# Kernel tuning notes

Hardware: AMD Instinct MI355X
Metric: run time of the kernel (lower is better)

Reference implementation:

```python
import jax, jax.numpy as jnp
import numpy as np

B_SZ, L_SEQ, H_CH, N_ST = 8, 4096, 256, 64


def setup_inputs() -> dict:
    key = jax.random.key(0)
    ks = jax.random.split(key, 12)
    rn = lambda k, s, sc=1.0: jax.random.normal(k, s, jnp.float32) * sc
    inp = {
        'x': rn(ks[0], (B_SZ, L_SEQ, H_CH)),
        # stable DPLR spectrum: Re(Lambda) < 0, HiPPO-like imaginary ladder
        'Lambda_re': -(jnp.abs(rn(ks[1], (N_ST,))) + 0.1),
        'Lambda_im': jnp.pi * jnp.arange(N_ST, dtype=jnp.float32),
        'P_re': rn(ks[2], (N_ST,), N_ST ** -0.5),
        'P_im': rn(ks[3], (N_ST,), N_ST ** -0.5),
        'Q_re': rn(ks[4], (N_ST,), N_ST ** -0.5),
        'Q_im': rn(ks[5], (N_ST,), N_ST ** -0.5),
        'B_re': rn(ks[6], (N_ST,), N_ST ** -0.5),
        'B_im': rn(ks[7], (N_ST,), N_ST ** -0.5),
        'C_re': rn(ks[8], (H_CH, N_ST), N_ST ** -0.5),
        'C_im': rn(ks[9], (H_CH, N_ST), N_ST ** -0.5),
        'step': jnp.ones((1,), jnp.float32) * 1e-3,
        'D': jnp.zeros((1,), jnp.float32),
        'W_fc': rn(ks[10], (H_CH, H_CH), H_CH ** -0.5),
        'b_fc': jnp.zeros((H_CH,), jnp.float32),
        'ln_g': jnp.ones((H_CH,), jnp.float32),
        'ln_b': jnp.zeros((H_CH,), jnp.float32),
    }
    return inp


def _dplr_kernel(Lambda_re, Lambda_im, P_re, P_im, Q_re, Q_im, B_re, B_im, C_re, C_im, step, L):
    # S4 DPLR generating function evaluated at the L roots of unity (torch_get_K_derta).
    Lam = (Lambda_re + 1j * Lambda_im).astype(jnp.complex64)  # (N,)
    Pc = (P_re + 1j * P_im).astype(jnp.complex64)
    Qc = (Q_re + 1j * Q_im).astype(jnp.complex64)
    Bc = (B_re + 1j * B_im).astype(jnp.complex64)
    Cc = (C_re + 1j * C_im).astype(jnp.complex64)  # (H, N)
    k = jnp.arange(L, dtype=jnp.float32)
    Omega = jnp.exp((-2j * jnp.pi) * (k / L)).astype(jnp.complex64)  # (L,)
    c = 2.0 / (1.0 + Omega)
    g = (2.0 / step[0]) * (1.0 - Omega) / (1.0 + Omega)  # bilinear transform points, (L,)
    inv = 1.0 / (g[:, None] - Lam[None, :])  # Cauchy matrix, (L, N)
    k00 = jnp.einsum('hn,ln->hl', Cc * Bc[None, :], inv)  # (H, L)
    k01 = jnp.einsum('hn,ln->hl', Cc * Pc[None, :], inv)
    k10 = jnp.einsum('n,ln->l', Qc * Bc, inv)  # (L,)
    k11 = jnp.einsum('n,ln->l', Qc * Pc, inv)
    atRoots = c[None, :] * (k00 - k01 * (k10 / (1.0 + k11))[None, :])  # Woodbury correction
    K = jnp.fft.ifft(atRoots, axis=-1).real  # (H, L)
    return K.astype(jnp.float32)


def reference(x, Lambda_re, Lambda_im, P_re, P_im, Q_re, Q_im, B_re, B_im, C_re, C_im, step, D, W_fc, b_fc, ln_g, ln_b):
    Bsz, L, H = x.shape
    step = jnp.maximum(step, 1e-6)
    K = _dplr_kernel(Lambda_re, Lambda_im, P_re, P_im, Q_re, Q_im, B_re, B_im, C_re, C_im, step, L)  # (H, L)
    # causal FFT convolution per channel (torch_convolution with fft=True)
    n = 2 * L
    Kf = jnp.fft.rfft(K, n=n, axis=-1)           # (H, F)
    uf = jnp.fft.rfft(x, n=n, axis=1)            # (B, F, H)
    h1 = jnp.fft.irfft(uf * Kf.T[None], n=n, axis=1)[:, :L, :]
    y1 = jax.nn.gelu(h1 + D * x, approximate=False)  # mult_activation='gelu'
    y2 = jax.nn.gelu(y1 @ W_fc.T + b_fc, approximate=False)  # fc + final_act
    y2 = y2 + x  # skip
    mu = jnp.mean(y2, axis=-1, keepdims=True)
    var = jnp.var(y2, axis=-1, keepdims=True)
    y = (y2 - mu) / jnp.sqrt(var + 1e-5) * ln_g + ln_b  # LayerNorm; dropout p=0
    h_ratio = jnp.max(jnp.abs(y), axis=1) / (jnp.max(jnp.abs(x), axis=1) + 1e-6)  # (B, H)
    return y, h_ratio
```

## Files before the change

kernel.cpp:

```cpp
#include <hip/hip_runtime.h>
#include <math.h>

#define TPB 256

typedef float2 cf;
typedef __attribute__((ext_vector_type(8))) short bf16x8;
typedef __attribute__((ext_vector_type(4))) float f32x4;

__device__ __forceinline__ cf cmk(float x, float y){ cf r; r.x=x; r.y=y; return r; }
__device__ __forceinline__ cf cml(cf a, cf b){ return cmk(a.x*b.x - a.y*b.y, a.x*b.y + a.y*b.x); }
__device__ __forceinline__ cf cad(cf a, cf b){ return cmk(a.x+b.x, a.y+b.y); }
__device__ __forceinline__ cf csb(cf a, cf b){ return cmk(a.x-b.x, a.y-b.y); }
__device__ __forceinline__ cf crcp(cf d){ float r = 1.0f/(d.x*d.x + d.y*d.y); return cmk(d.x*r, -d.y*r); }
__device__ __forceinline__ cf cdv(cf n, cf d){ return cml(n, crcp(d)); }
__device__ __forceinline__ float geluf(float z){ return 0.5f*z*(1.0f + erff(z*0.70710678118654752f)); }

__device__ __forceinline__ cf twid(float f, float sign){
  float h = f * 0.5f;
  float s = __builtin_amdgcn_sinf(h);
  float c0 = __builtin_amdgcn_cosf(h);
  return cmk(c0, sign * s);
}

__device__ __forceinline__ cf shflx(cf v, int m){
  return cmk(__shfl_xor(v.x, m), __shfl_xor(v.y, m));
}

__device__ __forceinline__ void bfsplit(float v, ushort* h, ushort* l){
  unsigned u = __float_as_uint(v);
  unsigned hr = (u + 0x7FFFu + ((u >> 16) & 1u)) & 0xFFFF0000u;
  *h = (ushort)(hr >> 16);
  float lv = v - __uint_as_float(hr);
  unsigned u2 = __float_as_uint(lv);
  *l = (ushort)((u2 + 0x7FFFu + ((u2 >> 16) & 1u)) >> 16);
}

__device__ __forceinline__ void dif4q(cf& q0, cf& q1, cf& q2, cf& q3, cf w1, float sign){
  cf w2 = cml(w1, w1);
  cf a1 = cad(q0, q2);
  cf c1 = cml(csb(q0, q2), w1);
  cf b1 = cad(q1, q3);
  cf d1 = cml(csb(q1, q3), cmk(-sign*w1.y, sign*w1.x));
  q0 = cad(a1, b1);
  q1 = cml(csb(a1, b1), w2);
  q2 = cad(c1, d1);
  q3 = cml(csb(c1, d1), w2);
}
__device__ __forceinline__ void dit4q(cf& q0, cf& q1, cf& q2, cf& q3, cf w1, float sign){
  cf w2 = cml(w1, w1);
  cf t1 = cml(q1, w2);
  cf a1 = cad(q0, t1), b1 = csb(q0, t1);
  cf t2 = cml(q3, w2);
  cf c1 = cad(q2, t2), d1 = csb(q2, t2);
  cf v1 = cml(c1, w1);
  cf v2 = cml(d1, cmk(-sign*w1.y, sign*w1.x));
  q0 = cad(a1, v1);
  q2 = csb(a1, v1);
  q1 = cad(b1, v2);
  q3 = csb(b1, v2);
}

template<int N, int SSTART>
__device__ void fft_dif_r4(cf* __restrict__ a, float sign){
  #pragma unroll
  for (int s = SSTART; s >= 1; s >>= 2){
    __syncthreads();
    #pragma unroll
    for (int g = 0; g < (N >> 2) / TPB; g++){
      int w = (int)threadIdx.x + g * TPB;
      int j = w & (s - 1);
      int base = ((w & ~(s - 1)) << 2) | j;
      cf A0 = a[base], B0 = a[base + s], C0 = a[base + 2*s], D0 = a[base + 3*s];
      cf w1 = twid((float)j / (float)(2 * s), sign);
      cf w2 = cml(w1, w1);
      cf a1 = cad(A0, C0);
      cf c1 = cml(csb(A0, C0), w1);
      cf b1 = cad(B0, D0);
      cf d1 = cml(csb(B0, D0), cmk(-sign * w1.y, sign * w1.x));
      a[base]         = cad(a1, b1);
      a[base + s]     = cml(csb(a1, b1), w2);
      a[base + 2*s]   = cad(c1, d1);
      a[base + 3*s]   = cml(csb(c1, d1), w2);
    }
  }
  if constexpr ((__builtin_ctz(N) & 1) == 1){
    __syncthreads();
    #pragma unroll
    for (int g = 0; g < (N >> 1) / TPB; g++){
      int w = (int)threadIdx.x + g * TPB;
      int i = w << 1;
      cf u = a[i], v = a[i + 1];
      a[i] = cad(u, v);
      a[i + 1] = csb(u, v);
    }
  }
  __syncthreads();
}

template<int N>
__device__ void fft_dit_r4(cf* __restrict__ a, float sign){
  if constexpr ((__builtin_ctz(N) & 1) == 1){
    __syncthreads();
    #pragma unroll
    for (int g = 0; g < (N >> 1) / TPB; g++){
      int w = (int)threadIdx.x + g * TPB;
      int i = w << 1;
      cf u = a[i], v = a[i + 1];
      a[i] = cad(u, v);
      a[i + 1] = csb(u, v);
    }
  }
  constexpr int S0 = ((__builtin_ctz(N) & 1) == 1) ? 2 : 1;
  #pragma unroll
  for (int s = S0; s <= (N >> 2); s <<= 2){
    __syncthreads();
    #pragma unroll
    for (int g = 0; g < (N >> 2) / TPB; g++){
      int w = (int)threadIdx.x + g * TPB;
      int j = w & (s - 1);
      int base = ((w & ~(s - 1)) << 2) | j;
      cf A0 = a[base], B0 = a[base + s], C0 = a[base + 2*s], D0 = a[base + 3*s];
      cf w1 = twid((float)j / (float)(2 * s), sign);
      cf w2 = cml(w1, w1);
      cf t1 = cml(B0, w2);
      cf a1 = cad(A0, t1), b1 = csb(A0, t1);
      cf t2 = cml(D0, w2);
      cf c1 = cad(C0, t2), d1 = csb(C0, t2);
      cf v1 = cml(c1, w1);
      cf v2 = cml(d1, cmk(-sign * w1.y, sign * w1.x));
      a[base]         = cad(a1, v1);
      a[base + 2*s]   = csb(a1, v1);
      a[base + s]     = cad(b1, v2);
      a[base + 3*s]   = csb(b1, v2);
    }
  }
  __syncthreads();
}

__device__ void dif8192_pad_stage(cf* __restrict__ a, float sign){
  __syncthreads();
  #pragma unroll
  for (int g = 0; g < 8; g++){
    int w = (int)threadIdx.x + g * TPB;
    cf A0 = a[w], B0 = a[w + 2048];
    cf w1 = twid((float)w * (1.0f / 4096.0f), sign);
    cf w2 = cml(w1, w1);
    cf c1 = cml(A0, w1);
    cf d1 = cml(B0, cmk(-sign * w1.y, sign * w1.x));
    a[w]        = cad(A0, B0);
    a[w + 2048] = cml(csb(A0, B0), w2);
    a[w + 4096] = cad(c1, d1);
    a[w + 6144] = cml(csb(c1, d1), w2);
  }
}

__device__ __forceinline__ int brev13(int x){ return (int)(__brev((unsigned)x) >> 19); }

__global__ void k_init(unsigned* xmax, unsigned* ymax){
  int i = blockIdx.x * 256 + threadIdx.x;
  if (i < 2048){ xmax[i] = 0u; ymax[i] = 0u; }
}

__global__ __launch_bounds__(256) void k_transpose_x(const float* __restrict__ x,
                                                     float* __restrict__ xT,
                                                     unsigned* __restrict__ xmax){
  __shared__ float tile[64][65];
  __shared__ float red[64][4];
  int b = blockIdx.z;
  int t0 = blockIdx.x * 64;
  int h0 = blockIdx.y * 64;
  int hc = threadIdx.x & 63, tg = threadIdx.x >> 6;
  float pmax = 0.0f;
  #pragma unroll
  for (int q = 0; q < 16; q++){
    int tr = tg + q * 4;
    float v = x[((size_t)(b * 4096 + t0 + tr)) * 256 + h0 + hc];
    tile[tr][hc] = v;
    pmax = fmaxf(pmax, fabsf(v));
  }
  red[hc][tg] = pmax;
  __syncthreads();
  if (threadIdx.x < 64){
    float m = fmaxf(fmaxf(red[threadIdx.x][0], red[threadIdx.x][1]),
                    fmaxf(red[threadIdx.x][2], red[threadIdx.x][3]));
    atomicMax(&xmax[b * 256 + h0 + threadIdx.x], __float_as_uint(m));
  }
  #pragma unroll
  for (int q = 0; q < 16; q++){
    int hr = tg + q * 4;
    xT[((size_t)(b * 256 + h0 + hr)) * 4096 + t0 + hc] = tile[hc][hr];
  }
}

__global__ void k_wsplit(const float* __restrict__ W, ushort* __restrict__ Wh, ushort* __restrict__ Wl){
  int i = blockIdx.x * 256 + threadIdx.x;
  ushort h, l;
  bfsplit(W[i], &h, &l);
  Wh[i] = h; Wl[i] = l;
}

__global__ __launch_bounds__(256) void k_cauchy(
    const float* __restrict__ Lr, const float* __restrict__ Li,
    const float* __restrict__ Pr, const float* __restrict__ Pi,
    const float* __restrict__ Qr, const float* __restrict__ Qi,
    const float* __restrict__ Br, const float* __restrict__ Bi,
    const float* __restrict__ Cr, const float* __restrict__ Ci,
    const float* __restrict__ stepp, cf* __restrict__ A)
{
  __shared__ cf sLam[64], sB[64], sP[64], sQB[64], sQP[64];
  __shared__ cf sInv[64][16];
  __shared__ cf sWood[16], sC[16], sG[16];
  int tid = threadIdx.x;
  int l0 = blockIdx.x * 16;
  float stepv = fmaxf(stepp[0], 1e-6f);
  if (tid < 64){
    cf lam = cmk(Lr[tid], Li[tid]);
    cf b = cmk(Br[tid], Bi[tid]);
    cf p = cmk(Pr[tid], Pi[tid]);
    cf q = cmk(Qr[tid], Qi[tid]);
    sLam[tid] = lam; sB[tid] = b; sP[tid] = p;
    sQB[tid] = cml(q, b);
    sQP[tid] = cml(q, p);
  }
  __syncthreads();
  if (tid < 16){
    int l = l0 + tid;
    float ang = -6.2831855f * ((float)l * (1.0f / 4096.0f));
    cf Om = cmk(cosf(ang), sinf(ang));
    cf den = cmk(1.0f + Om.x, Om.y);
    cf num = cmk(1.0f - Om.x, -Om.y);
    cf rden = crcp(den);
    sC[tid] = cml(cmk(2.0f, 0.0f), rden);
    cf g = cml(num, rden);
    float sc = 2.0f / stepv;
    sG[tid] = cmk(g.x * sc, g.y * sc);
  }
  __syncthreads();
  for (int it = tid; it < 1024; it += 256){
    int n = it >> 4, ll = it & 15;
    sInv[n][ll] = crcp(csb(sG[ll], sLam[n]));
  }
  __syncthreads();
  if (tid < 16){
    cf k10 = cmk(0,0), k11 = cmk(0,0);
    for (int n = 0; n < 64; n++){
      k10 = cad(k10, cml(sQB[n], sInv[n][tid]));
      k11 = cad(k11, cml(sQP[n], sInv[n][tid]));
    }
    sWood[tid] = cdv(k10, cmk(1.0f + k11.x, k11.y));
  }
  __syncthreads();
  int h = tid;
  cf a0[16], a1[16];
  #pragma unroll
  for (int ll = 0; ll < 16; ll++){ a0[ll] = cmk(0,0); a1[ll] = cmk(0,0); }
  for (int n = 0; n < 64; n++){
    cf cc = cmk(Cr[h * 64 + n], Ci[h * 64 + n]);
    cf cb = cml(cc, sB[n]);
    cf cp = cml(cc, sP[n]);
    #pragma unroll
    for (int ll = 0; ll < 16; ll++){
      cf iv = sInv[n][ll];
      a0[ll] = cad(a0[ll], cml(cb, iv));
      a1[ll] = cad(a1[ll], cml(cp, iv));
    }
  }
  cf* dst = A + (size_t)h * 4096 + l0;
  #pragma unroll
  for (int ll = 0; ll < 16; ll++){
    dst[ll] = cml(sC[ll], csb(a0[ll], cml(a1[ll], sWood[ll])));
  }
}

__global__ __launch_bounds__(256) void k_kf(const cf* __restrict__ A, float4* __restrict__ Sab){
  extern __shared__ cf c[];
  int hp = blockIdx.x, tid = threadIdx.x;
  const cf* a1p = A + (size_t)(2 * hp) * 4096;
  const cf* a2p = a1p + 4096;
  for (int l = tid; l < 4096; l += TPB){
    int r = (int)(__brev((unsigned)l) >> 20);
    cf u = a1p[l], v = a2p[l];
    c[r] = cmk(u.x - v.y, u.y + v.x);
  }
  fft_dit_r4<4096>(c, 1.0f);
  float k1[16], k2[16];
  #pragma unroll
  for (int q = 0; q < 16; q++){
    cf w = c[tid + q * 256];
    k1[q] = w.x * (1.0f / 4096.0f);
    k2[q] = w.y * (1.0f / 4096.0f);
  }
  __syncthreads();
  #pragma unroll
  for (int q = 0; q < 16; q++) c[tid + q * 256] = cmk(k1[q], k2[q]);
  dif8192_pad_stage(c, -1.0f);
  fft_dif_r4<8192, 512>(c, -1.0f);
  float4* rec = Sab + (size_t)hp * 4097;
  const float sc = 0.5f * 0.5f * (1.0f / 8192.0f);
  #pragma unroll
  for (int q8 = 0; q8 < 16; q8++){
    int t = tid + 256 * q8;
    int p = t << 1;
    int k = brev13(p);
    int qq = brev13((8192 - k) & 8191);
    cf Zp = c[p], Zq = c[qq];
    float K1x = (Zp.x + Zq.x), K1y = (Zp.y - Zq.y);
    float dx  = (Zp.x - Zq.x), dy  = (Zp.y + Zq.y);
    float K2x = dy, K2y = -dx;
    rec[t] = make_float4((K1x + K2x) * sc, (K1y + K2y) * sc,
                         (K1x - K2x) * sc, (K1y - K2y) * sc);
  }
  if (tid == 0){
    cf Z1 = c[1];
    float K1x = 2.0f * Z1.x, K2x = 2.0f * Z1.y;
    rec[4096] = make_float4((K1x + K2x) * sc, 0.0f, (K1x - K2x) * sc, 0.0f);
  }
}

__global__ __launch_bounds__(256) void k_conv(const float* __restrict__ xT,
                                              const float4* __restrict__ Sab,
                                              const float* __restrict__ Dp,
                                              ushort* __restrict__ y1h,
                                              ushort* __restrict__ y1l){
  __shared__ cf c[8320];
  int blk = blockIdx.x;
  int b = blk >> 7, hp = blk & 127;
  int t = threadIdx.x;
  const float* xs1 = xT + ((size_t)(b * 256 + 2 * hp)) * 4096;
  const float* xs2 = xs1 + 4096;
  cf v[32];
  #pragma unroll
  for (int r = 0; r < 16; r++){
    int n = t + 256 * r;
    v[r] = cmk(xs1[n], xs2[n]);
  }
  #pragma unroll
  for (int r = 0; r < 16; r++)
    v[r + 16] = cml(v[r], twid((float)(t + 256 * r) * (1.0f / 4096.0f), -1.0f));
  #pragma unroll
  for (int r0 = 0; r0 < 4; r0++){
    cf w1 = twid((float)(t + 256 * r0) * (1.0f / 2048.0f), -1.0f);
    dif4q(v[r0], v[r0 + 4], v[r0 + 8], v[r0 + 12], w1, -1.0f);
    dif4q(v[r0 + 16], v[r0 + 20], v[r0 + 24], v[r0 + 28], w1, -1.0f);
  }
  {
    cf w1 = twid((float)t * (1.0f / 512.0f), -1.0f);
    #pragma unroll
    for (int r = 0; r < 32; r += 4)
      dif4q(v[r], v[r + 1], v[r + 2], v[r + 3], w1, -1.0f);
  }
  #pragma unroll
  for (int r = 0; r < 32; r++) c[t + 260 * r] = v[r];
  __syncthreads();
  int Bq = t >> 3, sg = t & 7;
  int m1 = Bq * 260 + sg;
  #pragma unroll
  for (int u = 0; u < 32; u++) v[u] = c[m1 + 8 * u];
  #pragma unroll
  for (int u = 0; u < 8; u++){
    cf w1 = twid((float)(sg + 8 * u) * (1.0f / 128.0f), -1.0f);
    dif4q(v[u], v[u + 8], v[u + 16], v[u + 24], w1, -1.0f);
  }
  #pragma unroll
  for (int p2 = 0; p2 < 2; p2++){
    cf w1 = twid((float)(sg + 8 * p2) * (1.0f / 32.0f), -1.0f);
    #pragma unroll
    for (int u0 = 0; u0 < 32; u0 += 8)
      dif4q(v[u0 + p2], v[u0 + p2 + 2], v[u0 + p2 + 4], v[u0 + p2 + 6], w1, -1.0f);
  }
  {
    cf tw = twid((float)sg * (1.0f / 8.0f), -1.0f);
    #pragma unroll
    for (int u = 0; u < 32; u += 2){
      cf lo = cad(v[u], v[u + 1]);
      cf hi = cml(csb(v[u], v[u + 1]), tw);
      v[u] = lo; v[u + 1] = hi;
    }
  }
  {
    bool h4 = (sg & 4) != 0;
    cf tw4 = twid((float)(sg & 3) * 0.25f, -1.0f);
    #pragma unroll
    for (int u = 0; u < 32; u++){
      cf o = shflx(v[u], 4);
      v[u] = h4 ? cml(csb(o, v[u]), tw4) : cad(v[u], o);
    }
    bool h2 = (sg & 2) != 0;
    cf tw2 = twid((float)(sg & 1) * 0.5f, -1.0f);
    #pragma unroll
    for (int u = 0; u < 32; u++){
      cf o = shflx(v[u], 2);
      v[u] = h2 ? cml(csb(o, v[u]), tw2) : cad(v[u], o);
    }
    bool h1 = (sg & 1) != 0;
    #pragma unroll
    for (int u = 0; u < 32; u++){
      cf o = shflx(v[u], 1);
      v[u] = h1 ? csb(o, v[u]) : cad(v[u], o);
    }
  }
  #pragma unroll
  for (int u = 0; u < 32; u++) c[m1 + 8 * u] = v[u];
  __syncthreads();
  const float4* rec = Sab + (size_t)hp * 4097;
  #pragma unroll
  for (int q8 = 0; q8 < 16; q8++){
    int th = t + 256 * q8;
    int p = th << 1;
    int k = brev13(p);
    int qq = brev13((8192 - k) & 8191);
    int pi = p + 4 * (p >> 8), qi = qq + 4 * (qq >> 8);
    cf Zp = c[pi], Zq = c[qi];
    float4 r0 = rec[th];
    cf Sap = cmk(r0.x, r0.y), Sbp = cmk(r0.z, r0.w);
    cf cZq = cmk(Zq.x, -Zq.y), cZp = cmk(Zp.x, -Zp.y);
    c[pi] = cad(cml(Zp, Sap), cml(cZq, Sbp));
    cf cSa = cmk(Sap.x, -Sap.y), cSb = cmk(Sbp.x, -Sbp.y);
    c[qi] = cad(cml(Zq, cSa), cml(cZp, cSb));
  }
  if (t == 0){
    float4 e = rec[4096];
    cf Z1 = c[1];
    c[1] = cad(cml(Z1, cmk(e.x, e.y)), cml(cmk(Z1.x, -Z1.y), cmk(e.z, e.w)));
  }
  __syncthreads();
  #pragma unroll
  for (int u = 0; u < 32; u++) v[u] = c[m1 + 8 * u];
  {
    bool h1 = (sg & 1) != 0;
    #pragma unroll
    for (int u = 0; u < 32; u++){
      cf o = shflx(v[u], 1);
      v[u] = h1 ? csb(o, v[u]) : cad(v[u], o);
    }
    bool h2 = (sg & 2) != 0;
    cf w2 = twid((float)(sg & 1) * 0.5f, 1.0f);
    #pragma unroll
    for (int u = 0; u < 32; u++){
      cf o = shflx(v[u], 2);
      cf whv = cml(w2, h2 ? v[u] : o);
      v[u] = h2 ? csb(o, whv) : cad(v[u], whv);
    }
    bool h4 = (sg & 4) != 0;
    cf w4 = twid((float)(sg & 3) * 0.25f, 1.0f);
    #pragma unroll
    for (int u = 0; u < 32; u++){
      cf o = shflx(v[u], 4);
      cf whv = cml(w4, h4 ? v[u] : o);
      v[u] = h4 ? csb(o, whv) : cad(v[u], whv);
    }
  }
  {
    cf tw = twid((float)sg * (1.0f / 8.0f), 1.0f);
    #pragma unroll
    for (int u = 0; u < 32; u += 2){
      cf tb = cml(v[u + 1], tw);
      cf a = v[u];
      v[u] = cad(a, tb);
      v[u + 1] = csb(a, tb);
    }
  }
  #pragma unroll
  for (int p2 = 0; p2 < 2; p2++){
    cf w1 = twid((float)(sg + 8 * p2) * (1.0f / 32.0f), 1.0f);
    #pragma unroll
    for (int u0 = 0; u0 < 32; u0 += 8)
      dit4q(v[u0 + p2], v[u0 + p2 + 2], v[u0 + p2 + 4], v[u0 + p2 + 6], w1, 1.0f);
  }
  #pragma unroll
  for (int u = 0; u < 8; u++){
    cf w1 = twid((float)(sg + 8 * u) * (1.0f / 128.0f), 1.0f);
    dit4q(v[u], v[u + 8], v[u + 16], v[u + 24], w1, 1.0f);
  }
  #pragma unroll
  for (int u = 0; u < 32; u++) c[m1 + 8 * u] = v[u];
  __syncthreads();
  #pragma unroll
  for (int r = 0; r < 32; r++) v[r] = c[t + 260 * r];
  {
    cf tw = twid((float)t * (1.0f / 256.0f), 1.0f);
    #pragma unroll
    for (int r = 0; r < 32; r += 2){
      cf tb = cml(v[r + 1], tw);
      cf a = v[r];
      v[r] = cad(a, tb);
      v[r + 1] = csb(a, tb);
    }
  }
  #pragma unroll
  for (int p2 = 0; p2 < 2; p2++){
    cf w1 = twid((float)(t + 256 * p2) * (1.0f / 1024.0f), 1.0f);
    #pragma unroll
    for (int r0 = 0; r0 < 32; r0 += 8)
      dit4q(v[r0 + p2], v[r0 + p2 + 2], v[r0 + p2 + 4], v[r0 + p2 + 6], w1, 1.0f);
  }
  #pragma unroll
  for (int r0 = 0; r0 < 8; r0++){
    cf w1 = twid((float)(t + 256 * r0) * (1.0f / 4096.0f), 1.0f);
    dit4q(v[r0], v[r0 + 8], v[r0 + 16], v[r0 + 24], w1, 1.0f);
  }
  float Dv = Dp[0];
  size_t base = ((size_t)(b * 256 + 2 * hp)) * 4096;
  #pragma unroll
  for (int r = 0; r < 16; r++){
    int n = t + 256 * r;
    cf w = v[r];
    float z1 = geluf(fmaf(Dv, xs1[n], w.x));
    float z2 = geluf(fmaf(Dv, xs2[n], w.y));
    ushort h0, l0, h1u, l1;
    bfsplit(z1, &h0, &l0);
    bfsplit(z2, &h1u, &l1);
    y1h[base + n] = h0;        y1l[base + n] = l0;
    y1h[base + 4096 + n] = h1u; y1l[base + 4096 + n] = l1;
  }
}

__global__ __launch_bounds__(256, 3) void k_gemm_ln(
    const ushort* __restrict__ y1h, const ushort* __restrict__ y1l,
    const ushort* __restrict__ Wh, const ushort* __restrict__ Wl,
    const float* __restrict__ bfc, const float* __restrict__ x,
    const float* __restrict__ lng, const float* __restrict__ lnb,
    float* __restrict__ yout, unsigned* __restrict__ ymax)
{
  __shared__ ushort sY[2][64 * 40];
  __shared__ float red1[64][4], red2[64][4];
  int tid = threadIdx.x;
  int l = tid & 63;
  int w = tid >> 6;
  int blk = blockIdx.x;
  int b = blk >> 6;
  int t0 = (blk & 63) * 64;
  int g = l >> 4, cc = l & 15;

  f32x4 acc[4][4];
  #pragma unroll
  for (int m = 0; m < 4; m++)
    #pragma unroll
    for (int n = 0; n < 4; n++)
      acc[m][n] = (f32x4){0.0f, 0.0f, 0.0f, 0.0f};

  int kk = tid >> 3, ts = (tid & 7) * 8;

  #pragma unroll 1
  for (int kc = 0; kc < 256; kc += 32){
    __syncthreads();
    {
      size_t gb = ((size_t)(b * 256 + kc + kk)) * 4096 + t0 + ts;
      float4 vh = *(const float4*)(y1h + gb);
      float4 vl = *(const float4*)(y1l + gb);
      const ushort* ph = (const ushort*)&vh;
      const ushort* pl = (const ushort*)&vl;
      int kblk = kk >> 3, kin = kk & 7;
      #pragma unroll
      for (int e = 0; e < 8; e++){
        int t = ts + e;
        int idx = t * 40 + ((kblk ^ ((t >> 3) & 3)) << 3) + kin;
        sY[0][idx] = ph[e];
        sY[1][idx] = pl[e];
      }
    }
    __syncthreads();
    bf16x8 afh[4], afl[4];
    #pragma unroll
    for (int m = 0; m < 4; m++){
      int t = m * 16 + cc;
      int idx = t * 40 + ((g ^ ((t >> 3) & 3)) << 3);
      afh[m] = *(bf16x8*)&sY[0][idx];
      afl[m] = *(bf16x8*)&sY[1][idx];
    }
    #pragma unroll
    for (int n = 0; n < 4; n++){
      size_t wj = (size_t)(w * 64 + n * 16 + cc) * 256 + kc + g * 8;
      bf16x8 bh = *(const bf16x8*)(Wh + wj);
      bf16x8 bl = *(const bf16x8*)(Wl + wj);
      #pragma unroll
      for (int m = 0; m < 4; m++){
        acc[m][n] = __builtin_amdgcn_mfma_f32_16x16x32_bf16(afh[m], bh, acc[m][n], 0, 0, 0);
        acc[m][n] = __builtin_amdgcn_mfma_f32_16x16x32_bf16(afh[m], bl, acc[m][n], 0, 0, 0);
        acc[m][n] = __builtin_amdgcn_mfma_f32_16x16x32_bf16(afl[m], bh, acc[m][n], 0, 0, 0);
      }
    }
  }

  float bj[4], gj[4], lj[4];
  #pragma unroll
  for (int n = 0; n < 4; n++){
    int j = w * 64 + n * 16 + cc;
    bj[n] = bfc[j]; gj[n] = lng[j]; lj[n] = lnb[j];
  }
  #pragma unroll
  for (int m = 0; m < 4; m++){
    #pragma unroll
    for (int r = 0; r < 4; r++){
      int tl = m * 16 + g * 4 + r;
      size_t rowb = ((size_t)(b * 4096 + t0 + tl)) * 256;
      float ss = 0.0f, sq = 0.0f;
      #pragma unroll
      for (int n = 0; n < 4; n++){
        float z = geluf(acc[m][n][r] + bj[n]) + x[rowb + w * 64 + n * 16 + cc];
        acc[m][n][r] = z;
        ss += z; sq = fmaf(z, z, sq);
      }
      #pragma unroll
      for (int msk = 1; msk < 16; msk <<= 1){
        ss += __shfl_xor(ss, msk);
        sq += __shfl_xor(sq, msk);
      }
      if (cc == 0){ red1[tl][w] = ss; red2[tl][w] = sq; }
    }
  }
  __syncthreads();
  float jm[4] = {0.0f, 0.0f, 0.0f, 0.0f};
  #pragma unroll
  for (int m = 0; m < 4; m++){
    #pragma unroll
    for (int r = 0; r < 4; r++){
      int tl = m * 16 + g * 4 + r;
      float ts1 = red1[tl][0] + red1[tl][1] + red1[tl][2] + red1[tl][3];
      float ts2 = red2[tl][0] + red2[tl][1] + red2[tl][2] + red2[tl][3];
      float mu = ts1 * (1.0f / 256.0f);
      float var = ts2 * (1.0f / 256.0f) - mu * mu;
      float rstd = rsqrtf(var + 1e-5f);
      size_t rowb = ((size_t)(b * 4096 + t0 + tl)) * 256;
      #pragma unroll
      for (int n = 0; n < 4; n++){
        float yv = (acc[m][n][r] - mu) * rstd * gj[n] + lj[n];
        yout[rowb + w * 64 + n * 16 + cc] = yv;
        jm[n] = fmaxf(jm[n], fabsf(yv));
      }
    }
  }
  #pragma unroll
  for (int n = 0; n < 4; n++){
    jm[n] = fmaxf(jm[n], __shfl_xor(jm[n], 16));
    jm[n] = fmaxf(jm[n], __shfl_xor(jm[n], 32));
  }
  if (g == 0){
    #pragma unroll
    for (int n = 0; n < 4; n++)
      atomicMax(&ymax[b * 256 + w * 64 + n * 16 + cc], __float_as_uint(jm[n]));
  }
}

__global__ void k_ratio(const unsigned* __restrict__ ymax, const unsigned* __restrict__ xmax,
                        float* __restrict__ out){
  int i = blockIdx.x * 256 + threadIdx.x;
  if (i < 2048){
    float ym = __uint_as_float(ymax[i]);
    float xm = __uint_as_float(xmax[i]);
    out[8388608 + i] = ym / (xm + 1e-6f);
  }
}

extern "C" void kernel_launch(void* const* d_in, const int* in_sizes, int n_in,
                              void* d_out, int out_size, void* d_ws, size_t ws_size,
                              hipStream_t stream)
{
  const float* x    = (const float*)d_in[0];
  const float* Lr   = (const float*)d_in[1];
  const float* Li   = (const float*)d_in[2];
  const float* Pr   = (const float*)d_in[3];
  const float* Pi   = (const float*)d_in[4];
  const float* Qr   = (const float*)d_in[5];
  const float* Qi   = (const float*)d_in[6];
  const float* Br   = (const float*)d_in[7];
  const float* Bi   = (const float*)d_in[8];
  const float* Cr   = (const float*)d_in[9];
  const float* Ci   = (const float*)d_in[10];
  const float* stp  = (const float*)d_in[11];
  const float* Dp   = (const float*)d_in[12];
  const float* Wfc  = (const float*)d_in[13];
  const float* bfc  = (const float*)d_in[14];
  const float* lng  = (const float*)d_in[15];
  const float* lnb  = (const float*)d_in[16];

  char* ws = (char*)d_ws;
  float*    xT   = (float*)(ws);
  float4*   Sab  = (float4*)(ws + ((size_t)32 << 20));
  cf*       A    = (cf*)(ws + ((size_t)41 << 20));
  ushort*   y1h  = (ushort*)(ws + ((size_t)41 << 20));
  ushort*   y1l  = (ushort*)(ws + ((size_t)57 << 20));
  ushort*   Wh   = (ushort*)(ws + ((size_t)73 << 20));
  ushort*   Wl   = (ushort*)(ws + ((size_t)73 << 20) + (128u << 10));
  unsigned* xmax = (unsigned*)(ws + ((size_t)73 << 20) + (256u << 10));
  unsigned* ymax = xmax + 2048;

  k_init<<<8, 256, 0, stream>>>(xmax, ymax);
  dim3 gt(64, 4, 8);
  k_transpose_x<<<gt, 256, 0, stream>>>(x, xT, xmax);
  k_wsplit<<<256, 256, 0, stream>>>(Wfc, Wh, Wl);
  k_cauchy<<<256, 256, 0, stream>>>(Lr, Li, Pr, Pi, Qr, Qi, Br, Bi, Cr, Ci, stp, A);
  k_kf<<<128, 256, 65536, stream>>>(A, Sab);
  k_conv<<<1024, 256, 0, stream>>>(xT, Sab, Dp, y1h, y1l);
  k_gemm_ln<<<512, 256, 0, stream>>>(y1h, y1l, Wh, Wl, bfc, x, lng, lnb, (float*)d_out, ymax);
  k_ratio<<<8, 256, 0, stream>>>(ymax, xmax, (float*)d_out);
}
```

Baseline: 211.2 us.

## Split 8192-point padded FFT convolution into even/odd 4096-point halves

The convolution replaces the single 8192-point zero-padded FFT per channel pair with two 4096-point FFTs: one for the even frequency bins and one for the twiddled odd bins. The kernel spectra for the two halves are computed separately (S0 directly from the Cauchy values, Tt via a twiddled 4096 FFT), and the two inverse results are summed with an output twiddle. This halves the shared-memory footprint and register array per block so more blocks can be resident, at the cost of an extra kernel launch and two sequential smaller FFT passes.

Result: slower. 375.4 us (+77.8%).

```diff
diff --git a/kernel.cpp b/kernel.cpp
--- a/kernel.cpp
+++ b/kernel.cpp
@@ -11,6 +11,7 @@
 __device__ __forceinline__ cf cml(cf a, cf b){ return cmk(a.x*b.x - a.y*b.y, a.x*b.y + a.y*b.x); }
 __device__ __forceinline__ cf cad(cf a, cf b){ return cmk(a.x+b.x, a.y+b.y); }
 __device__ __forceinline__ cf csb(cf a, cf b){ return cmk(a.x-b.x, a.y-b.y); }
+__device__ __forceinline__ cf cjg(cf a){ return cmk(a.x, -a.y); }
 __device__ __forceinline__ cf crcp(cf d){ float r = 1.0f/(d.x*d.x + d.y*d.y); return cmk(d.x*r, -d.y*r); }
 __device__ __forceinline__ cf cdv(cf n, cf d){ return cml(n, crcp(d)); }
 __device__ __forceinline__ float geluf(float z){ return 0.5f*z*(1.0f + erff(z*0.70710678118654752f)); }
@@ -137,24 +138,137 @@
   __syncthreads();
 }
 
-__device__ void dif8192_pad_stage(cf* __restrict__ a, float sign){
-  __syncthreads();
-  #pragma unroll
-  for (int g = 0; g < 8; g++){
-    int w = (int)threadIdx.x + g * TPB;
-    cf A0 = a[w], B0 = a[w + 2048];
-    cf w1 = twid((float)w * (1.0f / 4096.0f), sign);
-    cf w2 = cml(w1, w1);
-    cf c1 = cml(A0, w1);
-    cf d1 = cml(B0, cmk(-sign * w1.y, sign * w1.x));
-    a[w]        = cad(A0, B0);
-    a[w + 2048] = cml(csb(A0, B0), w2);
-    a[w + 4096] = cad(c1, d1);
-    a[w + 6144] = cml(csb(c1, d1), w2);
-  }
-}
-
-__device__ __forceinline__ int brev13(int x){ return (int)(__brev((unsigned)x) >> 19); }
+__device__ __forceinline__ int brev12(int x){ return (int)(__brev((unsigned)x) >> 20); }
+
+
+__device__ __forceinline__ void dif4096_reg(cf (&v)[16], cf* __restrict__ c, int t, int lo){
+  #pragma unroll
+  for (int r0 = 0; r0 < 4; r0++){
+    cf w1 = twid((float)(t + 256*r0) * (1.0f/2048.0f), -1.0f);
+    dif4q(v[r0], v[r0+4], v[r0+8], v[r0+12], w1, -1.0f);
+  }
+  {
+    cf w1 = twid((float)t * (1.0f/512.0f), -1.0f);
+    #pragma unroll
+    for (int g = 0; g < 16; g += 4)
+      dif4q(v[g], v[g+1], v[g+2], v[g+3], w1, -1.0f);
+  }
+  __syncthreads();
+  #pragma unroll
+  for (int r = 0; r < 16; r++) c[t + 260*r] = v[r];
+  __syncthreads();
+  int m1 = (t >> 4) * 260 + lo;
+  #pragma unroll
+  for (int u = 0; u < 16; u++) v[u] = c[m1 + 16*u];
+  #pragma unroll
+  for (int u0 = 0; u0 < 4; u0++){
+    cf w1 = twid((float)(16*u0 + lo) * (1.0f/128.0f), -1.0f);
+    dif4q(v[u0], v[u0+4], v[u0+8], v[u0+12], w1, -1.0f);
+  }
+  {
+    cf w1 = twid((float)lo * (1.0f/32.0f), -1.0f);
+    #pragma unroll
+    for (int g = 0; g < 16; g += 4)
+      dif4q(v[g], v[g+1], v[g+2], v[g+3], w1, -1.0f);
+  }
+  {
+    bool h8 = (lo & 8) != 0;
+    cf tw8 = twid((float)(lo & 7) * 0.125f, -1.0f);
+    #pragma unroll
+    for (int u = 0; u < 16; u++){
+      cf o = shflx(v[u], 8);
+      v[u] = h8 ? cml(csb(o, v[u]), tw8) : cad(v[u], o);
+    }
+    bool h4 = (lo & 4) != 0;
+    cf tw4 = twid((float)(lo & 3) * 0.25f, -1.0f);
+    #pragma unroll
+    for (int u = 0; u < 16; u++){
+      cf o = shflx(v[u], 4);
+      v[u] = h4 ? cml(csb(o, v[u]), tw4) : cad(v[u], o);
+    }
+    bool h2 = (lo & 2) != 0;
+    cf tw2 = twid((float)(lo & 1) * 0.5f, -1.0f);
+    #pragma unroll
+    for (int u = 0; u < 16; u++){
+      cf o = shflx(v[u], 2);
+      v[u] = h2 ? cml(csb(o, v[u]), tw2) : cad(v[u], o);
+    }
+    bool h1 = (lo & 1) != 0;
+    #pragma unroll
+    for (int u = 0; u < 16; u++){
+      cf o = shflx(v[u], 1);
+      v[u] = h1 ? csb(o, v[u]) : cad(v[u], o);
+    }
+  }
+  #pragma unroll
+  for (int u = 0; u < 16; u++) c[m1 + 16*u] = v[u];
+  __syncthreads();
+}
+
+__device__ __forceinline__ void dit4096_reg(cf (&v)[16], cf* __restrict__ c, int t, int lo){
+  int m1 = (t >> 4) * 260 + lo;
+  #pragma unroll
+  for (int u = 0; u < 16; u++) v[u] = c[m1 + 16*u];
+  {
+    bool h1 = (lo & 1) != 0;
+    #pragma unroll
+    for (int u = 0; u < 16; u++){
+      cf o = shflx(v[u], 1);
+      v[u] = h1 ? csb(o, v[u]) : cad(v[u], o);
+    }
+    bool h2 = (lo & 2) != 0;
+    cf w2 = twid((float)(lo & 1) * 0.5f, 1.0f);
+    #pragma unroll
+    for (int u = 0; u < 16; u++){
+      cf o = shflx(v[u], 2);
+      cf whv = cml(w2, h2 ? v[u] : o);
+      v[u] = h2 ? csb(o, whv) : cad(v[u], whv);
+    }
+    bool h4 = (lo & 4) != 0;
+    cf w4 = twid((float)(lo & 3) * 0.25f, 1.0f);
+    #pragma unroll
+    for (int u = 0; u < 16; u++){
+      cf o = shflx(v[u], 4);
+      cf whv = cml(w4, h4 ? v[u] : o);
+      v[u] = h4 ? csb(o, whv) : cad(v[u], whv);
+    }
+    bool h8 = (lo & 8) != 0;
+    cf w8 = twid((float)(lo & 7) * 0.125f, 1.0f);
+    #pragma unroll
+    for (int u = 0; u < 16; u++){
+      cf o = shflx(v[u], 8);
+      cf whv = cml(w8, h8 ? v[u] : o);
+      v[u] = h8 ? csb(o, whv) : cad(v[u], whv);
+    }
+  }
+  {
+    cf w1 = twid((float)lo * (1.0f/32.0f), 1.0f);
+    #pragma unroll
+    for (int g = 0; g < 16; g += 4)
+      dit4q(v[g], v[g+1], v[g+2], v[g+3], w1, 1.0f);
+  }
+  #pragma unroll
+  for (int u0 = 0; u0 < 4; u0++){
+    cf w1 = twid((float)(16*u0 + lo) * (1.0f/128.0f), 1.0f);
+    dit4q(v[u0], v[u0+4], v[u0+8], v[u0+12], w1, 1.0f);
+  }
+  #pragma unroll
+  for (int u = 0; u < 16; u++) c[m1 + 16*u] = v[u];
+  __syncthreads();
+  #pragma unroll
+  for (int r = 0; r < 16; r++) v[r] = c[t + 260*r];
+  {
+    cf w1 = twid((float)t * (1.0f/512.0f), 1.0f);
+    #pragma unroll
+    for (int g = 0; g < 16; g += 4)
+      dit4q(v[g], v[g+1], v[g+2], v[g+3], w1, 1.0f);
+  }
+  #pragma unroll
+  for (int r0 = 0; r0 < 4; r0++){
+    cf w1 = twid((float)(t + 256*r0) * (1.0f/2048.0f), 1.0f);
+    dit4q(v[r0], v[r0+4], v[r0+8], v[r0+12], w1, 1.0f);
+  }
+}
 
 __global__ void k_init(unsigned* xmax, unsigned* ymax){
   int i = blockIdx.x * 256 + threadIdx.x;
@@ -272,245 +386,140 @@
   }
 }
 
-__global__ __launch_bounds__(256) void k_kf(const cf* __restrict__ A, float4* __restrict__ Sab){
+__global__ __launch_bounds__(256) void k_s0(const cf* __restrict__ A, float4* __restrict__ S0){
+  int hp = blockIdx.x;
+  int rec = blockIdx.y * 256 + threadIdx.x;
+  if (rec > 2048) return;
+  int k = (rec < 2048) ? brev12(rec << 1) : 2048;
+  int mk = (4096 - k) & 4095;
+  const cf* a1p = A + (size_t)(2 * hp) * 4096;
+  const cf* a2p = a1p + 4096;
+  cf K1 = cad(a1p[k], cjg(a1p[mk]));
+  cf K2 = cad(a2p[k], cjg(a2p[mk]));
+  const float s = 1.0f / 32768.0f;
+  S0[(size_t)hp * 2049 + rec] = make_float4((K1.x + K2.x) * s, (K1.y + K2.y) * s,
+                                            (K1.x - K2.x) * s, (K1.y - K2.y) * s);
+}
+
+__global__ __launch_bounds__(256) void k_kf(const cf* __restrict__ A, float4* __restrict__ Tt){
   extern __shared__ cf c[];
   int hp = blockIdx.x, tid = threadIdx.x;
   const cf* a1p = A + (size_t)(2 * hp) * 4096;
   const cf* a2p = a1p + 4096;
   for (int l = tid; l < 4096; l += TPB){
-    int r = (int)(__brev((unsigned)l) >> 20);
-    cf u = a1p[l], v = a2p[l];
-    c[r] = cmk(u.x - v.y, u.y + v.x);
+    int r = brev12(l);
+    cf u = a1p[l], w = a2p[l];
+    c[r] = cmk(u.x - w.y, u.y + w.x);
   }
   fft_dit_r4<4096>(c, 1.0f);
-  float k1[16], k2[16];
-  #pragma unroll
-  for (int q = 0; q < 16; q++){
-    cf w = c[tid + q * 256];
-    k1[q] = w.x * (1.0f / 4096.0f);
-    k2[q] = w.y * (1.0f / 4096.0f);
-  }
-  __syncthreads();
-  #pragma unroll
-  for (int q = 0; q < 16; q++) c[tid + q * 256] = cmk(k1[q], k2[q]);
-  dif8192_pad_stage(c, -1.0f);
-  fft_dif_r4<8192, 512>(c, -1.0f);
-  float4* rec = Sab + (size_t)hp * 4097;
-  const float sc = 0.5f * 0.5f * (1.0f / 8192.0f);
-  #pragma unroll
-  for (int q8 = 0; q8 < 16; q8++){
-    int t = tid + 256 * q8;
-    int p = t << 1;
-    int k = brev13(p);
-    int qq = brev13((8192 - k) & 8191);
-    cf Zp = c[p], Zq = c[qq];
-    float K1x = (Zp.x + Zq.x), K1y = (Zp.y - Zq.y);
-    float dx  = (Zp.x - Zq.x), dy  = (Zp.y + Zq.y);
-    float K2x = dy, K2y = -dx;
-    rec[t] = make_float4((K1x + K2x) * sc, (K1y + K2y) * sc,
-                         (K1x - K2x) * sc, (K1y - K2y) * sc);
-  }
-  if (tid == 0){
-    cf Z1 = c[1];
-    float K1x = 2.0f * Z1.x, K2x = 2.0f * Z1.y;
-    rec[4096] = make_float4((K1x + K2x) * sc, 0.0f, (K1x - K2x) * sc, 0.0f);
-  }
-}
-
-__global__ __launch_bounds__(256) void k_conv(const float* __restrict__ xT,
-                                              const float4* __restrict__ Sab,
-                                              const float* __restrict__ Dp,
-                                              ushort* __restrict__ y1h,
-                                              ushort* __restrict__ y1l){
-  __shared__ cf c[8320];
+  const float inv = 1.0f / 4096.0f;
+  for (int l = tid; l < 4096; l += TPB){
+    cf tw = twid((float)l * inv, -1.0f);
+    tw.x *= inv; tw.y *= inv;
+    c[l] = cml(c[l], tw);
+  }
+  fft_dif_r4<4096, 1024>(c, -1.0f);
+  float4* rec = Tt + (size_t)hp * 2048;
+  const float st = 1.0f / 32768.0f;
+  #pragma unroll
+  for (int q8 = 0; q8 < 8; q8++){
+    int tr = tid + 256 * q8;
+    int p = tr << 1;
+    int k = brev12(p);
+    int qs = brev12(4095 - k);
+    cf Zp = c[p], Zq = c[qs];
+    float G1x = Zp.x + Zq.x, G1y = Zp.y - Zq.y;
+    float dx = Zp.x - Zq.x, dy = Zp.y + Zq.y;
+    float G2x = dy, G2y = -dx;
+    rec[tr] = make_float4((G1x + G2x) * st, (G1y + G2y) * st,
+                          (G1x - G2x) * st, (G1y - G2y) * st);
+  }
+}
+
+__global__ __launch_bounds__(256, 4) void k_conv(const float* __restrict__ xT,
+                                                 const float4* __restrict__ S0,
+                                                 const float4* __restrict__ Tt,
+                                                 const float* __restrict__ Dp,
+                                                 ushort* __restrict__ y1h,
+                                                 ushort* __restrict__ y1l){
+  __shared__ cf c[4160];
   int blk = blockIdx.x;
   int b = blk >> 7, hp = blk & 127;
-  int t = threadIdx.x;
+  int t = threadIdx.x, lo = t & 15;
   const float* xs1 = xT + ((size_t)(b * 256 + 2 * hp)) * 4096;
   const float* xs2 = xs1 + 4096;
-  cf v[32];
+  cf xv[16], v[16];
   #pragma unroll
   for (int r = 0; r < 16; r++){
     int n = t + 256 * r;
-    v[r] = cmk(xs1[n], xs2[n]);
-  }
-  #pragma unroll
-  for (int r = 0; r < 16; r++)
-    v[r + 16] = cml(v[r], twid((float)(t + 256 * r) * (1.0f / 4096.0f), -1.0f));
-  #pragma unroll
-  for (int r0 = 0; r0 < 4; r0++){
-    cf w1 = twid((float)(t + 256 * r0) * (1.0f / 2048.0f), -1.0f);
-    dif4q(v[r0], v[r0 + 4], v[r0 + 8], v[r0 + 12], w1, -1.0f);
-    dif4q(v[r0 + 16], v[r0 + 20], v[r0 + 24], v[r0 + 28], w1, -1.0f);
-  }
+    xv[r] = cmk(xs1[n], xs2[n]);
+    v[r] = xv[r];
+  }
+  dif4096_reg(v, c, t, lo);
   {
-    cf w1 = twid((float)t * (1.0f / 512.0f), -1.0f);
-    #pragma unroll
-    for (int r = 0; r < 32; r += 4)
-      dif4q(v[r], v[r + 1], v[r + 2], v[r + 3], w1, -1.0f);
-  }
-  #pragma unroll
-  for (int r = 0; r < 32; r++) c[t + 260 * r] = v[r];
-  __syncthreads();
-  int Bq = t >> 3, sg = t & 7;
-  int m1 = Bq * 260 + sg;
-  #pragma unroll
-  for (int u = 0; u < 32; u++) v[u] = c[m1 + 8 * u];
-  #pragma unroll
-  for (int u = 0; u < 8; u++){
-    cf w1 = twid((float)(sg + 8 * u) * (1.0f / 128.0f), -1.0f);
-    dif4q(v[u], v[u + 8], v[u + 16], v[u + 24], w1, -1.0f);
-  }
-  #pragma unroll
-  for (int p2 = 0; p2 < 2; p2++){
-    cf w1 = twid((float)(sg + 8 * p2) * (1.0f / 32.0f), -1.0f);
-    #pragma unroll
-    for (int u0 = 0; u0 < 32; u0 += 8)
-      dif4q(v[u0 + p2], v[u0 + p2 + 2], v[u0 + p2 + 4], v[u0 + p2 + 6], w1, -1.0f);
-  }
+    const float4* rec0 = S0 + (size_t)hp * 2049;
+    #pragma unroll
+    for (int q8 = 0; q8 < 8; q8++){
+      int tr = t + 256 * q8;
+      int p = tr << 1;
+      int k = brev12(p);
+      int q0 = brev12((4096 - k) & 4095);
+      int pi = p + 4 * (p >> 8), qi = q0 + 4 * (q0 >> 8);
+      cf Zp = c[pi], Zq = c[qi];
+      float4 r0 = rec0[tr];
+      cf Sa = cmk(r0.x, r0.y), Sb = cmk(r0.z, r0.w);
+      c[pi] = cad(cml(Zp, Sa), cml(cjg(Zq), Sb));
+      c[qi] = cad(cml(Zq, cjg(Sa)), cml(cjg(Zp), cjg(Sb)));
+    }
+    if (t == 0){
+      float4 e = rec0[2048];
+      cf Z1 = c[1];
+      c[1] = cad(cml(Z1, cmk(e.x, e.y)), cml(cjg(Z1), cmk(e.z, e.w)));
+    }
+  }
+  __syncthreads();
+  dit4096_reg(v, c, t, lo);
+  cf acc[16];
+  #pragma unroll
+  for (int r = 0; r < 16; r++) acc[r] = v[r];
+  #pragma unroll
+  for (int r = 0; r < 16; r++){
+    int n = t + 256 * r;
+    v[r] = cml(xv[r], twid((float)n * (1.0f / 4096.0f), -1.0f));
+  }
+  dif4096_reg(v, c, t, lo);
   {
-    cf tw = twid((float)sg * (1.0f / 8.0f), -1.0f);
-    #pragma unroll
-    for (int u = 0; u < 32; u += 2){
-      cf lo = cad(v[u], v[u + 1]);
-      cf hi = cml(csb(v[u], v[u + 1]), tw);
-      v[u] = lo; v[u + 1] = hi;
-    }
-  }
-  {
-    bool h4 = (sg & 4) != 0;
-    cf tw4 = twid((float)(sg & 3) * 0.25f, -1.0f);
-    #pragma unroll
-    for (int u = 0; u < 32; u++){
-      cf o = shflx(v[u], 4);
-      v[u] = h4 ? cml(csb(o, v[u]), tw4) : cad(v[u], o);
-    }
-    bool h2 = (sg & 2) != 0;
-    cf tw2 = twid((float)(sg & 1) * 0.5f, -1.0f);
-    #pragma unroll
-    for (int u = 0; u < 32; u++){
-      cf o = shflx(v[u], 2);
-      v[u] = h2 ? cml(csb(o, v[u]), tw2) : cad(v[u], o);
-    }
-    bool h1 = (sg & 1) != 0;
-    #pragma unroll
-    for (int u = 0; u < 32; u++){
-      cf o = shflx(v[u], 1);
-      v[u] = h1 ? csb(o, v[u]) : cad(v[u], o);
-    }
-  }
-  #pragma unroll
-  for (int u = 0; u < 32; u++) c[m1 + 8 * u] = v[u];
-  __syncthreads();
-  const float4* rec = Sab + (size_t)hp * 4097;
-  #pragma unroll
-  for (int q8 = 0; q8 < 16; q8++){
-    int th = t + 256 * q8;
-    int p = th << 1;
-    int k = brev13(p);
-    int qq = brev13((8192 - k) & 8191);
-    int pi = p + 4 * (p >> 8), qi = qq + 4 * (qq >> 8);
-    cf Zp = c[pi], Zq = c[qi];
-    float4 r0 = rec[th];
-    cf Sap = cmk(r0.x, r0.y), Sbp = cmk(r0.z, r0.w);
-    cf cZq = cmk(Zq.x, -Zq.y), cZp = cmk(Zp.x, -Zp.y);
-    c[pi] = cad(cml(Zp, Sap), cml(cZq, Sbp));
-    cf cSa = cmk(Sap.x, -Sap.y), cSb = cmk(Sbp.x, -Sbp.y);
-    c[qi] = cad(cml(Zq, cSa), cml(cZp, cSb));
-  }
-  if (t == 0){
-    float4 e = rec[4096];
-    cf Z1 = c[1];
-    c[1] = cad(cml(Z1, cmk(e.x, e.y)), cml(cmk(Z1.x, -Z1.y), cmk(e.z, e.w)));
-  }
-  __syncthreads();
-  #pragma unroll
-  for (int u = 0; u < 32; u++) v[u] = c[m1 + 8 * u];
-  {
-    bool h1 = (sg & 1) != 0;
-    #pragma unroll
-    for (int u = 0; u < 32; u++){
-      cf o = shflx(v[u], 1);
-      v[u] = h1 ? csb(o, v[u]) : cad(v[u], o);
-    }
-    bool h2 = (sg & 2) != 0;
-    cf w2 = twid((float)(sg & 1) * 0.5f, 1.0f);
-    #pragma unroll
-    for (int u = 0; u < 32; u++){
-      cf o = shflx(v[u], 2);
-      cf whv = cml(w2, h2 ? v[u] : o);
-      v[u] = h2 ? csb(o, whv) : cad(v[u], whv);
-    }
-    bool h4 = (sg & 4) != 0;
-    cf w4 = twid((float)(sg & 3) * 0.25f, 1.0f);
-    #pragma unroll
-    for (int u = 0; u < 32; u++){
-      cf o = shflx(v[u], 4);
-      cf whv = cml(w4, h4 ? v[u] : o);
-      v[u] = h4 ? csb(o, whv) : cad(v[u], whv);
-    }
-  }
-  {
-    cf tw = twid((float)sg * (1.0f / 8.0f), 1.0f);
-    #pragma unroll
-    for (int u = 0; u < 32; u += 2){
-      cf tb = cml(v[u + 1], tw);
-      cf a = v[u];
-      v[u] = cad(a, tb);
-      v[u + 1] = csb(a, tb);
-    }
-  }
-  #pragma unroll
-  for (int p2 = 0; p2 < 2; p2++){
-    cf w1 = twid((float)(sg + 8 * p2) * (1.0f / 32.0f), 1.0f);
-    #pragma unroll
-    for (int u0 = 0; u0 < 32; u0 += 8)
-      dit4q(v[u0 + p2], v[u0 + p2 + 2], v[u0 + p2 + 4], v[u0 + p2 + 6], w1, 1.0f);
-  }
-  #pragma unroll
-  for (int u = 0; u < 8; u++){
-    cf w1 = twid((float)(sg + 8 * u) * (1.0f / 128.0f), 1.0f);
-    dit4q(v[u], v[u + 8], v[u + 16], v[u + 24], w1, 1.0f);
-  }
-  #pragma unroll
-  for (int u = 0; u < 32; u++) c[m1 + 8 * u] = v[u];
-  __syncthreads();
-  #pragma unroll
-  for (int r = 0; r < 32; r++) v[r] = c[t + 260 * r];
-  {
-    cf tw = twid((float)t * (1.0f / 256.0f), 1.0f);
-    #pragma unroll
-    for (int r = 0; r < 32; r += 2){
-      cf tb = cml(v[r + 1], tw);
-      cf a = v[r];
-      v[r] = cad(a, tb);
-      v[r + 1] = csb(a, tb);
-    }
-  }
-  #pragma unroll
-  for (int p2 = 0; p2 < 2; p2++){
-    cf w1 = twid((float)(t + 256 * p2) * (1.0f / 1024.0f), 1.0f);
-    #pragma unroll
-    for (int r0 = 0; r0 < 32; r0 += 8)
-      dit4q(v[r0 + p2], v[r0 + p2 + 2], v[r0 + p2 + 4], v[r0 + p2 + 6], w1, 1.0f);
-  }
-  #pragma unroll
-  for (int r0 = 0; r0 < 8; r0++){
-    cf w1 = twid((float)(t + 256 * r0) * (1.0f / 4096.0f), 1.0f);
-    dit4q(v[r0], v[r0 + 8], v[r0 + 16], v[r0 + 24], w1, 1.0f);
-  }
+    const float4* rec1 = Tt + (size_t)hp * 2048;
+    #pragma unroll
+    for (int q8 = 0; q8 < 8; q8++){
+      int tr = t + 256 * q8;
+      int p = tr << 1;
+      int k = brev12(p);
+      int q1 = brev12(4095 - k);
+      int pi = p + 4 * (p >> 8), qi = q1 + 4 * (q1 >> 8);
+      cf Zp = c[pi], Zq = c[qi];
+      float4 r0 = rec1[tr];
+      cf Ta = cmk(r0.x, r0.y), Tb = cmk(r0.z, r0.w);
+      c[pi] = cad(cml(Zp, Ta), cml(cjg(Zq), Tb));
+      c[qi] = cad(cml(Zq, cjg(Ta)), cml(cjg(Zp), cjg(Tb)));
+    }
+  }
+  __syncthreads();
+  dit4096_reg(v, c, t, lo);
   float Dv = Dp[0];
   size_t base = ((size_t)(b * 256 + 2 * hp)) * 4096;
   #pragma unroll
   for (int r = 0; r < 16; r++){
     int n = t + 256 * r;
-    cf w = v[r];
-    float z1 = geluf(fmaf(Dv, xs1[n], w.x));
-    float z2 = geluf(fmaf(Dv, xs2[n], w.y));
+    cf u = cml(v[r], twid((float)n * (1.0f / 4096.0f), 1.0f));
+    float y1 = acc[r].x + u.x;
+    float y2 = acc[r].y + u.y;
+    float z1 = geluf(fmaf(Dv, xs1[n], y1));
+    float z2 = geluf(fmaf(Dv, xs2[n], y2));
     ushort h0, l0, h1u, l1;
     bfsplit(z1, &h0, &l0);
     bfsplit(z2, &h1u, &l1);
-    y1h[base + n] = h0;        y1l[base + n] = l0;
+    y1h[base + n] = h0;         y1l[base + n] = l0;
     y1h[base + 4096 + n] = h1u; y1l[base + 4096 + n] = l1;
   }
 }
@@ -676,7 +685,8 @@
 
   char* ws = (char*)d_ws;
   float*    xT   = (float*)(ws);
-  float4*   Sab  = (float4*)(ws + ((size_t)32 << 20));
+  float4*   S0   = (float4*)(ws + ((size_t)32 << 20));
+  float4*   Tt   = (float4*)(ws + ((size_t)36 << 20) + (512u << 10));
   cf*       A    = (cf*)(ws + ((size_t)41 << 20));
   ushort*   y1h  = (ushort*)(ws + ((size_t)41 << 20));
   ushort*   y1l  = (ushort*)(ws + ((size_t)57 << 20));
@@ -690,8 +700,9 @@
   k_transpose_x<<<gt, 256, 0, stream>>>(x, xT, xmax);
   k_wsplit<<<256, 256, 0, stream>>>(Wfc, Wh, Wl);
   k_cauchy<<<256, 256, 0, stream>>>(Lr, Li, Pr, Pi, Qr, Qi, Br, Bi, Cr, Ci, stp, A);
-  k_kf<<<128, 256, 65536, stream>>>(A, Sab);
-  k_conv<<<1024, 256, 0, stream>>>(xT, Sab, Dp, y1h, y1l);
+  k_s0<<<dim3(128, 9), 256, 0, stream>>>(A, S0);
+  k_kf<<<128, 256, 32768, stream>>>(A, Tt);
+  k_conv<<<1024, 256, 0, stream>>>(xT, S0, Tt, Dp, y1h, y1l);
   k_gemm_ln<<<512, 256, 0, stream>>>(y1h, y1l, Wh, Wl, bfc, x, lng, lnb, (float*)d_out, ymax);
   k_ratio<<<8, 256, 0, stream>>>(ymax, xmax, (float*)d_out);
 }
```
